# Kernel tuning notes

Measured on AMD Instinct MI355X. Metric: run time of the kernel, lower is better.

Reference implementation:

```python
import jax, jax.numpy as jnp
import numpy as np

N = 100000        # nodes
E = 1600000       # random edges (self-loops appended in setup)
IN = 128          # in_channels
HID = 32          # hidden_channels per head
HEADS = 4         # num_heads
OUT = 64          # out_channels (final layer, 1 head)
HH = HID * HEADS  # head_hidden_dim = 128
NEG_SLOPE = 0.2   # PyG GATConv leaky_relu slope


def setup_inputs() -> dict:
    key = jax.random.key(0)
    ks = jax.random.split(key, 20)
    x = jax.random.normal(ks[0], (N, IN), jnp.float32)
    src = jax.random.randint(ks[1], (E,), 0, N)
    dst = jax.random.randint(ks[2], (E,), 0, N)
    loop = jnp.arange(N)  # self-loops (GATConv add_self_loops=True)
    edge_index = jnp.stack([jnp.concatenate([src, loop]),
                            jnp.concatenate([dst, loop])]).astype(jnp.int32)
    counts = jnp.zeros((N, 1), jnp.float32)  # unused (use_counts=False)
    g = lambda k, sh: (jax.random.normal(k, sh, jnp.float32) * 0.05)
    inp = {
        "x": x, "counts": counts,
        "enc_w": g(ks[3], (IN, HH)), "enc_b": jnp.zeros((HH,), jnp.float32),
        # layer 1: HH -> HEADS*HID
        "W1": g(ks[4], (HH, HEADS * HID)), "as1": g(ks[5], (HEADS, HID)),
        "ad1": g(ks[6], (HEADS, HID)), "b1": jnp.zeros((HEADS * HID,), jnp.float32),
        # layer 2: HH -> HEADS*HID
        "W2": g(ks[7], (HH, HEADS * HID)), "as2": g(ks[8], (HEADS, HID)),
        "ad2": g(ks[9], (HEADS, HID)), "b2": jnp.zeros((HEADS * HID,), jnp.float32),
        # layer 3: HH -> 1*OUT
        "W3": g(ks[10], (HH, OUT)), "as3": g(ks[11], (1, OUT)),
        "ad3": g(ks[12], (1, OUT)), "b3": jnp.zeros((OUT,), jnp.float32),
        "edge_index": edge_index,
        "use_counts": 0,
    }
    return inp


def gat_conv(x, W, a_src, a_dst, bias, src, dst, heads, ch):
    # h: [N, heads, ch] per-head projected features
    h = (x @ W).reshape(-1, heads, ch)
    es = jnp.einsum('nhc,hc->nh', h, a_src)   # alpha_src per node
    ed = jnp.einsum('nhc,hc->nh', h, a_dst)   # alpha_dst per node
    e = jax.nn.leaky_relu(es[src] + ed[dst], NEG_SLOPE)  # [E, heads]
    # softmax over incoming edges of each dst node (segment softmax)
    m = jax.ops.segment_max(e, dst, num_segments=N)
    ex = jnp.exp(e - m[dst])
    den = jax.ops.segment_sum(ex, dst, num_segments=N)
    alpha = ex / den[dst]                     # self-loops guarantee den > 0
    out = jax.ops.segment_sum(h[src] * alpha[:, :, None], dst, num_segments=N)
    return out.reshape(-1, heads * ch) + bias


def reference(x, counts, enc_w, enc_b, W1, as1, ad1, b1, W2, as2, ad2, b2,
              W3, as3, ad3, b3, edge_index, use_counts):
    # use_counts=False path: x = encode_h(x)
    src, dst = edge_index[0], edge_index[1]
    h = x @ enc_w + enc_b
    h = gat_conv(h, W1, as1, ad1, b1, src, dst, HEADS, HID)
    h = jax.nn.relu(h)  # dropout is identity in eval mode
    h = gat_conv(h, W2, as2, ad2, b2, src, dst, HEADS, HID)
    h = jax.nn.relu(h)
    h = gat_conv(h, W3, as3, ad3, b3, src, dst, 1, OUT)
    return h
```

## Files before the change

### kernel.cpp

```cpp
#include <hip/hip_runtime.h>
#include <hip/hip_fp16.h>


template <int OUTC, bool BIAS, int NH, bool HOUT>
__global__ __launch_bounds__(256) void gemm_k(const float* __restrict__ X,
                                              const float* __restrict__ W,
                                              const float* __restrict__ B,
                                              const float* __restrict__ AS,
                                              const float* __restrict__ AD,
                                              float* __restrict__ es,
                                              float* __restrict__ ed,
                                              float* __restrict__ Y,
                                              __half* __restrict__ Hh, int n) {
  __shared__ float sW[32 * OUTC];
  __shared__ float sX[32 * 128];
  int row0 = blockIdx.x * 32;
  for (int i = threadIdx.x * 4; i < 32 * 128; i += 256 * 4) {
    int r = i >> 7, c = i & 127;
    int gr = row0 + r;
    float4 v = make_float4(0.f, 0.f, 0.f, 0.f);
    if (gr < n) v = *(const float4*)&X[(size_t)gr * 128 + c];
    *(float4*)&sX[i] = v;
  }
  const int tx = threadIdx.x & 31;
  const int ty = threadIdx.x >> 5;
  constexpr int CPT = OUTC / 32;
  const int c0 = tx * CPT;
  const int r0 = ty * 4;
  float acc[4][CPT];
#pragma unroll
  for (int r = 0; r < 4; r++)
#pragma unroll
    for (int c = 0; c < CPT; c++) acc[r][c] = 0.f;

  for (int kc = 0; kc < 128; kc += 32) {
    __syncthreads();
    for (int i = threadIdx.x * 4; i < 32 * OUTC; i += 256 * 4)
      *(float4*)&sW[i] = *(const float4*)&W[kc * OUTC + i];
    __syncthreads();
#pragma unroll 2
    for (int kk4 = 0; kk4 < 32; kk4 += 4) {
      int k = kc + kk4;
      float4 xv0 = *(float4*)&sX[(r0 + 0) * 128 + k];
      float4 xv1 = *(float4*)&sX[(r0 + 1) * 128 + k];
      float4 xv2 = *(float4*)&sX[(r0 + 2) * 128 + k];
      float4 xv3 = *(float4*)&sX[(r0 + 3) * 128 + k];
#pragma unroll
      for (int kk = 0; kk < 4; kk++) {
        float w[CPT];
#pragma unroll
        for (int c = 0; c < CPT; c++) w[c] = sW[(kk4 + kk) * OUTC + c0 + c];
        float x0 = (&xv0.x)[kk], x1 = (&xv1.x)[kk], x2 = (&xv2.x)[kk], x3 = (&xv3.x)[kk];
#pragma unroll
        for (int c = 0; c < CPT; c++) {
          acc[0][c] = fmaf(x0, w[c], acc[0][c]);
          acc[1][c] = fmaf(x1, w[c], acc[1][c]);
          acc[2][c] = fmaf(x2, w[c], acc[2][c]);
          acc[3][c] = fmaf(x3, w[c], acc[3][c]);
        }
      }
    }
  }
  if constexpr (BIAS) {
#pragma unroll
    for (int r = 0; r < 4; r++)
#pragma unroll
      for (int c = 0; c < CPT; c++) acc[r][c] += B[c0 + c];
  }
#pragma unroll
  for (int r = 0; r < 4; r++) {
    int gr = row0 + r0 + r;
    if (gr < n) {
      if constexpr (HOUT) {
        __half2 p0 = __floats2half2_rn(acc[r][0], acc[r][1]);
        __half2 p1 = __floats2half2_rn(acc[r][2], acc[r][3]);
        uint2 pk;
        pk.x = *reinterpret_cast<unsigned*>(&p0);
        pk.y = *reinterpret_cast<unsigned*>(&p1);
        *(uint2*)&Hh[(size_t)gr * OUTC + c0] = pk;
      } else {
#pragma unroll
        for (int c = 0; c < CPT; c++)
          Y[(size_t)gr * OUTC + c0 + c] = acc[r][c];
      }
    }
  }
  if constexpr (NH > 0) {
    constexpr int CH = OUTC / NH;
    constexpr int GRP = CH / CPT;
    float asv[CPT], adv[CPT];
#pragma unroll
    for (int c = 0; c < CPT; c++) { asv[c] = AS[c0 + c]; adv[c] = AD[c0 + c]; }
#pragma unroll
    for (int r = 0; r < 4; r++) {
      float ps = 0.f, pd = 0.f;
#pragma unroll
      for (int c = 0; c < CPT; c++) {
        ps = fmaf(acc[r][c], asv[c], ps);
        pd = fmaf(acc[r][c], adv[c], pd);
      }
#pragma unroll
      for (int off = 1; off < GRP; off <<= 1) {
        ps += __shfl_xor(ps, off, 64);
        pd += __shfl_xor(pd, off, 64);
      }
      int gr = row0 + r0 + r;
      if (gr < n && (tx & (GRP - 1)) == 0) {
        int hh = tx / GRP;
        es[(size_t)gr * NH + hh] = ps;
        ed[(size_t)gr * NH + hh] = pd;
      }
    }
  }
}

__global__ __launch_bounds__(256) void wfold_k(const float* __restrict__ EW,
                                               const float* __restrict__ W1,
                                               const float* __restrict__ EB,
                                               float* __restrict__ Weff,
                                               float* __restrict__ beff) {
  if (blockIdx.x == 16) {
    int c = threadIdx.x;
    if (c < 128) {
      float acc = 0.f;
      for (int k = 0; k < 128; k++) acc = fmaf(EB[k], W1[k * 128 + c], acc);
      beff[c] = acc;
    }
    return;
  }
  int row = blockIdx.x * 8 + (threadIdx.x >> 5);
  int c0 = (threadIdx.x & 31) * 4;
  float4 acc = make_float4(0.f, 0.f, 0.f, 0.f);
  for (int k = 0; k < 128; k++) {
    float xv = EW[row * 128 + k];
    float4 wv = *(const float4*)&W1[k * 128 + c0];
    acc.x = fmaf(xv, wv.x, acc.x);
    acc.y = fmaf(xv, wv.y, acc.y);
    acc.z = fmaf(xv, wv.z, acc.z);
    acc.w = fmaf(xv, wv.w, acc.w);
  }
  *(float4*)&Weff[row * 128 + c0] = acc;
}

__global__ __launch_bounds__(256) void rank_k(const int* __restrict__ dst,
                                              int* __restrict__ cnt,
                                              int* __restrict__ rank, int ET) {
  int e = blockIdx.x * 256 + threadIdx.x;
  if (e < ET) rank[e] = atomicAdd(&cnt[dst[e]], 1);
}

__global__ __launch_bounds__(256) void block_scan_k(const int* __restrict__ cnt,
                                                    int* __restrict__ row_ptr,
                                                    int* __restrict__ bsum, int n) {
  __shared__ int s[256];
  int t = threadIdx.x;
  int idx = blockIdx.x * 256 + t;
  int val = (idx < n) ? cnt[idx] : 0;
  s[t] = val;
  __syncthreads();
  for (int off = 1; off < 256; off <<= 1) {
    int x = (t >= off) ? s[t - off] : 0;
    __syncthreads();
    s[t] += x;
    __syncthreads();
  }
  if (idx < n) row_ptr[idx] = s[t] - val;
  if (t == 255) bsum[blockIdx.x] = s[255];
}

__global__ __launch_bounds__(512) void bsum_scan_k(int* __restrict__ bsum, int nb) {
  __shared__ int s[512];
  int t = threadIdx.x;
  int v = (t < nb) ? bsum[t] : 0;
  s[t] = v;
  __syncthreads();
  for (int off = 1; off < 512; off <<= 1) {
    int x = (t >= off) ? s[t - off] : 0;
    __syncthreads();
    s[t] += x;
    __syncthreads();
  }
  if (t < nb) bsum[t] = s[t] - v;
}

__global__ __launch_bounds__(256) void add_off_k(int* __restrict__ row_ptr,
                                                 const int* __restrict__ bsum,
                                                 int n, int ET) {
  int idx = blockIdx.x * 256 + threadIdx.x;
  if (idx < n) row_ptr[idx] += bsum[idx >> 8];
  if (idx == 0) row_ptr[n] = ET;
}

__global__ __launch_bounds__(256) void fill_k(const int* __restrict__ src,
                                              const int* __restrict__ dst,
                                              const int* __restrict__ row_ptr,
                                              const int* __restrict__ rank,
                                              int* __restrict__ csr_src, int ET) {
  int e = blockIdx.x * 256 + threadIdx.x;
  if (e >= ET) return;
  csr_src[row_ptr[dst[e]] + rank[e]] = src[e];
}

template <int NH, bool RELU, bool HALF>
__global__ __launch_bounds__(256) void aggr_csr_k(const void* __restrict__ Hrow,
                                                  const float* __restrict__ es,
                                                  const float* __restrict__ ed,
                                                  const int* __restrict__ row_ptr,
                                                  const int* __restrict__ csr_src,
                                                  const float* __restrict__ bias,
                                                  float* __restrict__ out, int n) {
  constexpr int NC = HALF ? 128 : 64;
  constexpr int CPL = HALF ? 8 : 4;

  const int g = threadIdx.x >> 4;
  const int d = blockIdx.x * 16 + g;
  if (d >= n) return;
  const int gl = threadIdx.x & 15;
  const int ch0 = gl * CPL;
  const int head = (NH == 4) ? (ch0 >> 5) : 0;
  const int beg = row_ptr[d];
  const int deg = row_ptr[d + 1] - beg;
  const float ed_h = ed[(size_t)d * NH + head];
  const char* __restrict__ Hb = (const char*)Hrow;

  float den = 0.f;
  float a[CPL];
#pragma unroll
  for (int c = 0; c < CPL; c++) a[c] = 0.f;

  auto loadE = [&](int idx, float& e, uint4& h) {
    bool valid = idx < deg;
    int ii = valid ? beg + idx : beg;
    int ss = csr_src[ii];
    e = valid ? es[(size_t)ss * NH + head] : -1e30f;
    h = *(const uint4*)(Hb + (size_t)ss * 256 + gl * 16);
  };
  auto consume = [&](float e, const uint4& h) {
    float vv = e + ed_h;
    vv = vv >= 0.f ? vv : 0.2f * vv;
    float ex = __expf(vv);
    den += ex;
    if constexpr (HALF) {
      const unsigned* u = &h.x;
#pragma unroll
      for (int q = 0; q < 4; q++) {
        __half2 h2 = *reinterpret_cast<const __half2*>(&u[q]);
        float2 f2 = __half22float2(h2);
        a[2 * q]     = fmaf(f2.x, ex, a[2 * q]);
        a[2 * q + 1] = fmaf(f2.y, ex, a[2 * q + 1]);
      }
    } else {
      const float4 f = *reinterpret_cast<const float4*>(&h);
      a[0] = fmaf(f.x, ex, a[0]);
      a[1] = fmaf(f.y, ex, a[1]);
      a[2] = fmaf(f.z, ex, a[2]);
      a[3] = fmaf(f.w, ex, a[3]);
    }
  };

  float eA, eB;
  uint4 hA, hB;
  loadE(0, eA, hA);
  loadE(1, eB, hB);
  for (int i = 0; i < deg; i += 2) {
    float eA2 = -1e30f, eB2 = -1e30f;
    uint4 hA2 = make_uint4(0, 0, 0, 0), hB2 = hA2;
    if (i + 2 < deg) {
      loadE(i + 2, eA2, hA2);
      loadE(i + 3, eB2, hB2);
    }
    consume(eA, hA);
    consume(eB, hB);
    eA = eA2; hA = hA2;
    eB = eB2; hB = hB2;
  }

  float inv = 1.f / den;
#pragma unroll
  for (int q = 0; q < CPL / 4; q++) {
    float4 bv = *(const float4*)&bias[ch0 + 4 * q];
    float4 o;
    o.x = fmaf(a[4 * q + 0], inv, bv.x);
    o.y = fmaf(a[4 * q + 1], inv, bv.y);
    o.z = fmaf(a[4 * q + 2], inv, bv.z);
    o.w = fmaf(a[4 * q + 3], inv, bv.w);
    if (RELU) {
      o.x = fmaxf(o.x, 0.f); o.y = fmaxf(o.y, 0.f);
      o.z = fmaxf(o.z, 0.f); o.w = fmaxf(o.w, 0.f);
    }
    *(float4*)&out[(size_t)d * NC + ch0 + 4 * q] = o;
  }
}

extern "C" void kernel_launch(void* const* d_in, const int* in_sizes, int n_in,
                              void* d_out, int out_size, void* d_ws, size_t ws_size,
                              hipStream_t stream) {
  const float* x = (const float*)d_in[0];
  const float* encw = (const float*)d_in[2];
  const float* encb = (const float*)d_in[3];
  const float* W1 = (const float*)d_in[4];
  const float* as1 = (const float*)d_in[5];
  const float* ad1 = (const float*)d_in[6];
  const float* b1 = (const float*)d_in[7];
  const float* W2 = (const float*)d_in[8];
  const float* as2 = (const float*)d_in[9];
  const float* ad2 = (const float*)d_in[10];
  const float* b2 = (const float*)d_in[11];
  const float* W3 = (const float*)d_in[12];
  const float* as3 = (const float*)d_in[13];
  const float* ad3 = (const float*)d_in[14];
  const float* b3 = (const float*)d_in[15];
  const int* ei = (const int*)d_in[16];

  const int N_ = in_sizes[0] / 128;
  const int ET = in_sizes[16] / 2;
  const int* srcp = ei;
  const int* dstp = ei + ET;
  float* out = (float*)d_out;

  size_t NB = (size_t)N_ * 128 * sizeof(float);
  char* p = (char*)d_ws;
  float* bufA = (float*)p;      p += NB;
  float* bufB = (float*)p;      p += NB;
  __half* Hh = (__half*)bufB;
  int* rank = (int*)bufB;
  float* es = (float*)p;        p += (size_t)N_ * 4 * sizeof(float);
  float* ed = (float*)p;        p += (size_t)N_ * 4 * sizeof(float);
  int* cnt = (int*)p;           p += (size_t)N_ * sizeof(int);
  int* row_ptr = (int*)p;       p += (size_t)(N_ + 1) * sizeof(int);
  int* bsum = (int*)p;          p += (size_t)((N_ + 255) / 256) * sizeof(int);
  int* csr_src = (int*)p;       p += (size_t)ET * sizeof(int);
  float* Weff = (float*)p;      p += (size_t)128 * 128 * sizeof(float);
  float* beff = (float*)p;      p += (size_t)128 * sizeof(float);

  dim3 b256(256);
  int gGemm = (N_ + 31) / 32;
  int gNode = (N_ + 255) / 256;
  int gEdge = (ET + 255) / 256;
  int gAggr = (N_ + 15) / 16;
  int nb = (N_ + 255) / 256;

  wfold_k<<<17, b256, 0, stream>>>(encw, W1, encb, Weff, beff);
  hipMemsetAsync(cnt, 0, (size_t)N_ * sizeof(int), stream);
  rank_k<<<gEdge, b256, 0, stream>>>(dstp, cnt, rank, ET);
  block_scan_k<<<nb, b256, 0, stream>>>(cnt, row_ptr, bsum, N_);
  bsum_scan_k<<<1, 512, 0, stream>>>(bsum, nb);
  add_off_k<<<gNode, b256, 0, stream>>>(row_ptr, bsum, N_, ET);
  fill_k<<<gEdge, b256, 0, stream>>>(srcp, dstp, row_ptr, rank, csr_src, ET);

  gemm_k<128, true, 4, true><<<gGemm, b256, 0, stream>>>(x, Weff, beff, as1, ad1,
                                                         es, ed, nullptr, Hh, N_);
  aggr_csr_k<4, true, true><<<gAggr, b256, 0, stream>>>(Hh, es, ed, row_ptr,
                                                        csr_src, b1, bufA, N_);

  gemm_k<128, false, 4, true><<<gGemm, b256, 0, stream>>>(bufA, W2, nullptr, as2, ad2,
                                                          es, ed, nullptr, Hh, N_);
  aggr_csr_k<4, true, true><<<gAggr, b256, 0, stream>>>(Hh, es, ed, row_ptr,
                                                        csr_src, b2, bufA, N_);

  gemm_k<64, false, 1, false><<<gGemm, b256, 0, stream>>>(bufA, W3, nullptr, as3, ad3,
                                                          es, ed, bufB, nullptr, N_);
  aggr_csr_k<1, false, false><<<gAggr, b256, 0, stream>>>(bufB, es, ed, row_ptr,
                                                          csr_src, b3, out, N_);
}
```

Baseline: 609.9 us.

## Use fp16 MFMA for the two 128-wide GAT projection GEMMs

```diff
diff --git a/kernel.cpp b/kernel.cpp
--- a/kernel.cpp
+++ b/kernel.cpp
@@ -2,7 +2,107 @@
 #include <hip/hip_fp16.h>
 
 
-template <int OUTC, bool BIAS, int NH, bool HOUT>
+typedef _Float16 half8_t __attribute__((ext_vector_type(8)));
+typedef float f32x4_t __attribute__((ext_vector_type(4)));
+
+template <bool BIAS>
+__global__ __launch_bounds__(256) void gemm_mfma_k(const float* __restrict__ X,
+                                                   const __half* __restrict__ Wt,
+                                                   const float* __restrict__ B,
+                                                   const float* __restrict__ AS,
+                                                   const float* __restrict__ AD,
+                                                   float* __restrict__ es,
+                                                   float* __restrict__ ed,
+                                                   __half* __restrict__ Hh, int n) {
+  __shared__ __half sX[32 * 136];
+  __shared__ __half sWt[128 * 136];
+  const int row0 = blockIdx.x * 32;
+
+  for (int i = threadIdx.x * 4; i < 32 * 128; i += 1024) {
+    int r = i >> 7, c = i & 127;
+    int gr = row0 + r;
+    float4 v = make_float4(0.f, 0.f, 0.f, 0.f);
+    if (gr < n) v = *(const float4*)&X[(size_t)gr * 128 + c];
+    __half2 p0 = __floats2half2_rn(v.x, v.y);
+    __half2 p1 = __floats2half2_rn(v.z, v.w);
+    uint2 pk;
+    pk.x = *reinterpret_cast<unsigned*>(&p0);
+    pk.y = *reinterpret_cast<unsigned*>(&p1);
+    *(uint2*)&sX[r * 136 + c] = pk;
+  }
+  for (int i = threadIdx.x * 8; i < 128 * 128; i += 2048) {
+    int c = i >> 7, k = i & 127;
+    *(uint4*)&sWt[c * 136 + k] = *(const uint4*)&Wt[i];
+  }
+  __syncthreads();
+
+  const int l = threadIdx.x & 63;
+  const int wv = threadIdx.x >> 6;
+  const int mh = wv & 1;
+  const int nq = wv >> 1;
+  const int lrow = l & 15;
+  const int kg = l >> 4;
+
+  f32x4_t acc[4];
+#pragma unroll
+  for (int nt = 0; nt < 4; nt++) acc[nt] = (f32x4_t){0.f, 0.f, 0.f, 0.f};
+
+#pragma unroll
+  for (int ks = 0; ks < 4; ks++) {
+    half8_t af = *(const half8_t*)&sX[(mh * 16 + lrow) * 136 + ks * 32 + kg * 8];
+#pragma unroll
+    for (int nt = 0; nt < 4; nt++) {
+      int col = nq * 64 + nt * 16 + lrow;
+      half8_t bf = *(const half8_t*)&sWt[col * 136 + ks * 32 + kg * 8];
+      acc[nt] = __builtin_amdgcn_mfma_f32_16x16x32_f16(af, bf, acc[nt], 0, 0, 0);
+    }
+  }
+
+  float asv[4], adv[4];
+#pragma unroll
+  for (int nt = 0; nt < 4; nt++) {
+    int col = nq * 64 + nt * 16 + lrow;
+    if (BIAS) {
+      float bv = B[col];
+#pragma unroll
+      for (int r = 0; r < 4; r++) acc[nt][r] += bv;
+    }
+    asv[nt] = AS[col];
+    adv[nt] = AD[col];
+  }
+
+#pragma unroll
+  for (int r = 0; r < 4; r++) {
+    int gr = row0 + mh * 16 + kg * 4 + r;
+    if (gr < n) {
+#pragma unroll
+      for (int nt = 0; nt < 4; nt++) {
+        int col = nq * 64 + nt * 16 + lrow;
+        Hh[(size_t)gr * 128 + col] = __float2half(acc[nt][r]);
+      }
+    }
+  }
+#pragma unroll
+  for (int hs = 0; hs < 2; hs++) {
+#pragma unroll
+    for (int r = 0; r < 4; r++) {
+      float ps = acc[2 * hs][r] * asv[2 * hs] + acc[2 * hs + 1][r] * asv[2 * hs + 1];
+      float pd = acc[2 * hs][r] * adv[2 * hs] + acc[2 * hs + 1][r] * adv[2 * hs + 1];
+#pragma unroll
+      for (int off = 1; off < 16; off <<= 1) {
+        ps += __shfl_xor(ps, off, 64);
+        pd += __shfl_xor(pd, off, 64);
+      }
+      int gr = row0 + mh * 16 + kg * 4 + r;
+      if (lrow == 0 && gr < n) {
+        es[(size_t)gr * 4 + nq * 2 + hs] = ps;
+        ed[(size_t)gr * 4 + nq * 2 + hs] = pd;
+      }
+    }
+  }
+}
+
+template <int OUTC, bool BIAS, int NH>
 __global__ __launch_bounds__(256) void gemm_k(const float* __restrict__ X,
                                               const float* __restrict__ W,
                                               const float* __restrict__ B,
@@ -10,8 +110,7 @@
                                               const float* __restrict__ AD,
                                               float* __restrict__ es,
                                               float* __restrict__ ed,
-                                              float* __restrict__ Y,
-                                              __half* __restrict__ Hh, int n) {
+                                              float* __restrict__ Y, int n) {
   __shared__ float sW[32 * OUTC];
   __shared__ float sX[32 * 128];
   int row0 = blockIdx.x * 32;
@@ -71,18 +170,9 @@
   for (int r = 0; r < 4; r++) {
     int gr = row0 + r0 + r;
     if (gr < n) {
-      if constexpr (HOUT) {
-        __half2 p0 = __floats2half2_rn(acc[r][0], acc[r][1]);
-        __half2 p1 = __floats2half2_rn(acc[r][2], acc[r][3]);
-        uint2 pk;
-        pk.x = *reinterpret_cast<unsigned*>(&p0);
-        pk.y = *reinterpret_cast<unsigned*>(&p1);
-        *(uint2*)&Hh[(size_t)gr * OUTC + c0] = pk;
-      } else {
-#pragma unroll
-        for (int c = 0; c < CPT; c++)
-          Y[(size_t)gr * OUTC + c0 + c] = acc[r][c];
-      }
+#pragma unroll
+      for (int c = 0; c < CPT; c++)
+        Y[(size_t)gr * OUTC + c0 + c] = acc[r][c];
     }
   }
   if constexpr (NH > 0) {
@@ -140,6 +230,15 @@
     acc.w = fmaf(xv, wv.w, acc.w);
   }
   *(float4*)&Weff[row * 128 + c0] = acc;
+}
+
+__global__ __launch_bounds__(256) void wtrans_k(const float* __restrict__ W,
+                                                __half* __restrict__ Wt) {
+  int idx = blockIdx.x * 256 + threadIdx.x;
+  if (idx < 128 * 128) {
+    int c = idx >> 7, k = idx & 127;
+    Wt[idx] = __float2half(W[k * 128 + c]);
+  }
 }
 
 __global__ __launch_bounds__(256) void rank_k(const int* __restrict__ dst,
@@ -332,6 +431,8 @@
   int* csr_src = (int*)p;       p += (size_t)ET * sizeof(int);
   float* Weff = (float*)p;      p += (size_t)128 * 128 * sizeof(float);
   float* beff = (float*)p;      p += (size_t)128 * sizeof(float);
+  __half* Wefft = (__half*)p;   p += (size_t)128 * 128 * sizeof(__half);
+  __half* W2t = (__half*)p;     p += (size_t)128 * 128 * sizeof(__half);
 
   dim3 b256(256);
   int gGemm = (N_ + 31) / 32;
@@ -341,6 +442,8 @@
   int nb = (N_ + 255) / 256;
 
   wfold_k<<<17, b256, 0, stream>>>(encw, W1, encb, Weff, beff);
+  wtrans_k<<<64, b256, 0, stream>>>(Weff, Wefft);
+  wtrans_k<<<64, b256, 0, stream>>>(W2, W2t);
   hipMemsetAsync(cnt, 0, (size_t)N_ * sizeof(int), stream);
   rank_k<<<gEdge, b256, 0, stream>>>(dstp, cnt, rank, ET);
   block_scan_k<<<nb, b256, 0, stream>>>(cnt, row_ptr, bsum, N_);
@@ -348,18 +451,18 @@
   add_off_k<<<gNode, b256, 0, stream>>>(row_ptr, bsum, N_, ET);
   fill_k<<<gEdge, b256, 0, stream>>>(srcp, dstp, row_ptr, rank, csr_src, ET);
 
-  gemm_k<128, true, 4, true><<<gGemm, b256, 0, stream>>>(x, Weff, beff, as1, ad1,
-                                                         es, ed, nullptr, Hh, N_);
+  gemm_mfma_k<true><<<gGemm, b256, 0, stream>>>(x, Wefft, beff, as1, ad1,
+                                                es, ed, Hh, N_);
   aggr_csr_k<4, true, true><<<gAggr, b256, 0, stream>>>(Hh, es, ed, row_ptr,
                                                         csr_src, b1, bufA, N_);
 
-  gemm_k<128, false, 4, true><<<gGemm, b256, 0, stream>>>(bufA, W2, nullptr, as2, ad2,
-                                                          es, ed, nullptr, Hh, N_);
+  gemm_mfma_k<false><<<gGemm, b256, 0, stream>>>(bufA, W2t, nullptr, as2, ad2,
+                                                 es, ed, Hh, N_);
   aggr_csr_k<4, true, true><<<gAggr, b256, 0, stream>>>(Hh, es, ed, row_ptr,
                                                         csr_src, b2, bufA, N_);
 
-  gemm_k<64, false, 1, false><<<gGemm, b256, 0, stream>>>(bufA, W3, nullptr, as3, ad3,
-                                                          es, ed, bufB, nullptr, N_);
+  gemm_k<64, false, 1><<<gGemm, b256, 0, stream>>>(bufA, W3, nullptr, as3, ad3,
+                                                   es, ed, bufB, N_);
   aggr_csr_k<1, false, false><<<gAggr, b256, 0, stream>>>(bufB, es, ed, row_ptr,
                                                           csr_src, b3, out, N_);
 }
```

After: 565.7 us. -7.2%, faster.
